# Kernel tuning notes

Measured on AMD Instinct MI355X. Metric: run time of the kernel, lower is better.

## Reference

```python
import jax, jax.numpy as jnp
import numpy as np

B, NODE, DEG, K = 16, 32, 64, 8
IN_F, OUT_F, SUP = 128, 3, 10
FEATS = [96, 256, 256, 256, 128, 128]
SIZES = [1, 2, 4, 8, 16, 32]


def setup_inputs() -> dict:
    key = jax.random.key(0)
    ks = jax.random.split(key, 20)
    d = {}
    for i in range(6):
        d[f"t{i}"] = jax.random.normal(ks[i], (B, SIZES[i], FEATS[i]), jnp.float32)
    for i in range(6):
        d[f"Wr{i}"] = jax.random.normal(ks[6 + i], (FEATS[i], OUT_F), jnp.float32) * 0.1
    d["W_branch"] = jax.random.normal(ks[12], (NODE, IN_F, DEG * IN_F), jnp.float32) * 0.02
    d["Wl1"] = jax.random.normal(ks[13], (IN_F, IN_F * SUP), jnp.float32) * 0.05
    d["Wl2"] = jax.random.normal(ks[14], (IN_F * SUP, OUT_F), jnp.float32) * 0.02
    d["bias"] = jax.random.uniform(ks[15], (1, DEG, OUT_F), jnp.float32, -0.5, 0.5)
    d["c1w"] = jax.random.normal(ks[16], (64, 6), jnp.float32) * 0.2
    d["c1b"] = jnp.zeros((64,), jnp.float32)
    d["c2w"] = jax.random.normal(ks[17], (3, 64), jnp.float32) * 0.1
    d["c2b"] = jnp.zeros((3,), jnp.float32)
    return d


def _leaky(x):
    return jnp.where(x >= 0, x, 0.2 * x)  # LeakyReLU(0.2)


def reference(t0, t1, t2, t3, t4, t5, Wr0, Wr1, Wr2, Wr3, Wr4, Wr5,
              W_branch, Wl1, Wl2, bias, c1w, c1b, c2w, c2b):
    trees = [t0, t1, t2, t3, t4, t5]
    Wrs = [Wr0, Wr1, Wr2, Wr3, Wr4, Wr5]

    # --- root aggregation: per-ancestor linear + contiguous tiling to `node` rows ---
    root = jnp.zeros((B, NODE, OUT_F), jnp.float32)
    for t, W in zip(trees, Wrs):
        rn = t.shape[1]
        root = root + jnp.repeat(t @ W, NODE // rn, axis=1)  # (B, NODE, 3)

    # --- branch upsample: per-node weight matrix, then 2-layer loop MLP ---
    branch = _leaky(jnp.einsum('bni,nio->bno', t5, W_branch))  # (B, NODE, DEG*IN_F)
    branch = branch.reshape(B, NODE * DEG, IN_F)
    branch = (branch @ Wl1) @ Wl2  # (B, N, 3)
    branch = jnp.repeat(root, DEG, axis=1) + branch  # (B, N, 3), N = NODE*DEG

    # --- EdgeConv: knn on 3-d points, gather, 1x1 convs, max over neighbors ---
    x = branch  # (B, N, 3) point coordinates
    xx = jnp.sum(x * x, axis=-1)  # (B, N)
    inner = jnp.einsum('bnc,bmc->bnm', x, x)  # (B, N, N)
    pd = 2.0 * inner - xx[:, :, None] - xx[:, None, :]  # -squared distance
    _, idx = jax.lax.top_k(pd, K)  # (B, N, K) nearest-neighbor indices

    feat = x[jnp.arange(B)[:, None, None], idx]  # (B, N, K, 3) gather
    center = jnp.broadcast_to(x[:, :, None, :], feat.shape)
    g = jnp.concatenate([feat - center, center], axis=-1)  # (B, N, K, 6)

    h = jnp.einsum('bnkc,oc->bnko', g, c1w) + c1b  # conv1 1x1: 6 -> 64
    h = jnp.einsum('bnko,po->bnkp', h, c2w) + c2b  # conv2 1x1: 64 -> 3
    h = jnp.max(h, axis=2)  # max over K neighbors -> (B, N, 3)

    out = _leaky(h + jnp.tile(bias, (1, NODE, 1)))  # bias (1, DEG, 3) tiled to (1, N, 3)
    return out
```

## Files before the change

kernel.cpp:

```cpp
#include <hip/hip_runtime.h>
#include <float.h>

#define B_    16
#define NODE_ 32
#define DEG_  64
#define KNN_  8
#define INF_  128
#define ROWS_ 2048
#define JDIM_ 8192

#define OFF_X     0
#define OFF_Y     131072
#define OFF_ROOT  (OFF_Y + 4194304)
#define OFF_WL12  (OFF_ROOT + 2048)
#define OFF_EFF   (OFF_WL12 + 512)

__device__ __forceinline__ float med3f(float a, float b, float c) {
    return __builtin_amdgcn_fmed3f(a, b, c);
}
__device__ __forceinline__ float leaky(float v) { return v >= 0.f ? v : 0.2f * v; }

__global__ __launch_bounds__(128) void kA(
    const float* __restrict__ t0, const float* __restrict__ t1, const float* __restrict__ t2,
    const float* __restrict__ t3, const float* __restrict__ t4, const float* __restrict__ t5,
    const float* __restrict__ Wr0, const float* __restrict__ Wr1, const float* __restrict__ Wr2,
    const float* __restrict__ Wr3, const float* __restrict__ Wr4, const float* __restrict__ Wr5,
    const float* __restrict__ Wl1, const float* __restrict__ Wl2,
    const float* __restrict__ c1w, const float* __restrict__ c1b,
    const float* __restrict__ c2w, const float* __restrict__ c2b,
    float* __restrict__ ws)
{
    const int blk = blockIdx.x, tid = threadIdx.x;
    if (blk == 0) {
        const float* wp = Wl1 + tid * 1280;
        float a0 = 0.f, a1 = 0.f, a2 = 0.f;
        for (int s = 0; s < 1280; ++s) {
            float w = wp[s];
            a0 = fmaf(w, Wl2[s * 3 + 0], a0);
            a1 = fmaf(w, Wl2[s * 3 + 1], a1);
            a2 = fmaf(w, Wl2[s * 3 + 2], a2);
        }
        float* o = ws + OFF_WL12 + tid * 4;
        o[0] = a0; o[1] = a1; o[2] = a2; o[3] = 0.f;
    } else if (blk <= 12) {
        int idx = (blk - 1) * 128 + tid;
        int c = idx % 3, n = (idx / 3) & 31, b = idx / 96;
        float acc = 0.f;
#define TREE(T, W, RN, F) { \
        const float* tp = T + (b * RN + ((n * RN) >> 5)) * F; \
        for (int k = 0; k < F; ++k) acc = fmaf(tp[k], W[k * 3 + c], acc); }
        TREE(t0, Wr0, 1, 96)
        TREE(t1, Wr1, 2, 256)
        TREE(t2, Wr2, 4, 256)
        TREE(t3, Wr3, 8, 256)
        TREE(t4, Wr4, 16, 128)
        TREE(t5, Wr5, 32, 128)
#undef TREE
        ws[OFF_ROOT + (b * 32 + n) * 4 + c] = acc;
    } else {
        if (tid < 18) {
            int p = tid / 6, c = tid % 6;
            float a = 0.f;
            for (int o = 0; o < 64; ++o) a = fmaf(c2w[p * 64 + o], c1w[o * 6 + c], a);
            ws[OFF_EFF + tid] = a;
        } else if (tid < 21) {
            int p = tid - 18;
            float a = c2b[p];
            for (int o = 0; o < 64; ++o) a = fmaf(c2w[p * 64 + o], c1b[o], a);
            ws[OFF_EFF + 24 + p] = a;
        }
    }
}

__global__ __launch_bounds__(256) void kB1(const float* __restrict__ t5,
                                           const float* __restrict__ Wb,
                                           float* __restrict__ ws)
{
    const int n = blockIdx.x >> 5, jt = blockIdx.x & 31, tid = threadIdx.x;
    __shared__ float ts[128 * 16];
    for (int q = tid; q < 2048; q += 256) {
        int b = q >> 7, k = q & 127;
        ts[k * 16 + b] = t5[b * 4096 + n * 128 + k];
    }
    __syncthreads();
    const int j = jt * 256 + tid;
    const float* wp = Wb + n * 1048576 + j;
    float acc[16];
#pragma unroll
    for (int b = 0; b < 16; ++b) acc[b] = 0.f;
#pragma unroll 4
    for (int k = 0; k < 128; ++k) {
        float w = wp[k * 8192];
        const float4* tk = (const float4*)(ts + (k << 4));
        float4 a0 = tk[0], a1 = tk[1], a2 = tk[2], a3 = tk[3];
        acc[0]  = fmaf(a0.x, w, acc[0]);  acc[1]  = fmaf(a0.y, w, acc[1]);
        acc[2]  = fmaf(a0.z, w, acc[2]);  acc[3]  = fmaf(a0.w, w, acc[3]);
        acc[4]  = fmaf(a1.x, w, acc[4]);  acc[5]  = fmaf(a1.y, w, acc[5]);
        acc[6]  = fmaf(a1.z, w, acc[6]);  acc[7]  = fmaf(a1.w, w, acc[7]);
        acc[8]  = fmaf(a2.x, w, acc[8]);  acc[9]  = fmaf(a2.y, w, acc[9]);
        acc[10] = fmaf(a2.z, w, acc[10]); acc[11] = fmaf(a2.w, w, acc[11]);
        acc[12] = fmaf(a3.x, w, acc[12]); acc[13] = fmaf(a3.y, w, acc[13]);
        acc[14] = fmaf(a3.z, w, acc[14]); acc[15] = fmaf(a3.w, w, acc[15]);
    }
    float* yp = ws + OFF_Y + n * 8192 + j;
#pragma unroll
    for (int b = 0; b < 16; ++b) yp[b * 262144] = leaky(acc[b]);
}

__global__ __launch_bounds__(256) void kB2(float* __restrict__ ws)
{
    __shared__ float wl[512];
    const int tid = threadIdx.x;
    for (int q = tid; q < 512; q += 256) wl[q] = ws[OFF_WL12 + q];
    __syncthreads();
    const int gid = blockIdx.x * 256 + tid;
    const int b = gid >> 11, r = gid & 2047, n = r >> 6;
    const float* rt = ws + OFF_ROOT + ((b * 32 + n) << 2);
    float x0 = rt[0], x1 = rt[1], x2 = rt[2];
    const float4* yp = (const float4*)(ws + OFF_Y + (size_t)(b * 32 + n) * 8192 + ((r & 63) << 7));
#pragma unroll 8
    for (int i4 = 0; i4 < 32; ++i4) {
        float4 y = yp[i4];
        const float4* wr = ((const float4*)wl) + (i4 << 2);
        float4 w0 = wr[0], w1 = wr[1], w2 = wr[2], w3 = wr[3];
        x0 = fmaf(y.x, w0.x, x0); x0 = fmaf(y.y, w1.x, x0); x0 = fmaf(y.z, w2.x, x0); x0 = fmaf(y.w, w3.x, x0);
        x1 = fmaf(y.x, w0.y, x1); x1 = fmaf(y.y, w1.y, x1); x1 = fmaf(y.z, w2.y, x1); x1 = fmaf(y.w, w3.y, x1);
        x2 = fmaf(y.x, w0.z, x2); x2 = fmaf(y.y, w1.z, x2); x2 = fmaf(y.z, w2.z, x2); x2 = fmaf(y.w, w3.z, x2);
    }
    float xx = fmaf(x0, x0, fmaf(x1, x1, x2 * x2));
    ((float4*)(ws + OFF_X))[gid] = make_float4(x0, x1, x2, xx);
}

#define CAP_ 16
#define CSWAPD(a, b) { float _hi = fmaxf(a, b), _lo = fminf(a, b); a = _hi; b = _lo; }
__global__ __launch_bounds__(256) void kC(const float* __restrict__ ws,
                                          const float* __restrict__ bias,
                                          float* __restrict__ out)
{
    const int bb = blockIdx.x >> 6, rtile = blockIdx.x & 63, tid = threadIdx.x;
    __shared__ float4 xs[2048];
    __shared__ float eff[32];
    __shared__ int cnt[32];
    __shared__ int lists[32][CAP_];
    __shared__ int sel[32][KNN_];

    const float4* xg = (const float4*)(ws + OFF_X) + bb * 2048;
    for (int q = tid; q < 2048; q += 256) xs[q] = xg[q];
    if (tid < 32) { eff[tid] = ws[OFF_EFF + tid]; cnt[tid] = 0; }
    __syncthreads();

    const int lr = tid >> 3;
    const int part = tid & 7;
    const int r = rtile * 32 + lr;
    const float4 xr = xs[r];

    float s0 = -FLT_MAX, s1 = -FLT_MAX, s2 = -FLT_MAX, s3 = -FLT_MAX;
    float s4 = -FLT_MAX, s5 = -FLT_MAX, s6 = -FLT_MAX, s7 = -FLT_MAX;
#pragma unroll 4
    for (int mm = 0; mm < 256; ++mm) {
        float4 xm = xs[(mm << 3) | part];
        float dot = fmaf(xr.x, xm.x, fmaf(xr.y, xm.y, xr.z * xm.z));
        float pd = fmaf(2.f, dot, -(xr.w + xm.w));
        s7 = med3f(pd, s7, s6); s6 = med3f(pd, s6, s5);
        s5 = med3f(pd, s5, s4); s4 = med3f(pd, s4, s3);
        s3 = med3f(pd, s3, s2); s2 = med3f(pd, s2, s1);
        s1 = med3f(pd, s1, s0); s0 = fmaxf(s0, pd);
    }
#pragma unroll
    for (int w = 1; w < 8; w <<= 1) {
        float o0 = __shfl_xor(s0, w), o1 = __shfl_xor(s1, w), o2 = __shfl_xor(s2, w), o3 = __shfl_xor(s3, w);
        float o4 = __shfl_xor(s4, w), o5 = __shfl_xor(s5, w), o6 = __shfl_xor(s6, w), o7 = __shfl_xor(s7, w);
        float n0 = fmaxf(s0, o7), n1 = fmaxf(s1, o6), n2 = fmaxf(s2, o5), n3 = fmaxf(s3, o4);
        float n4 = fmaxf(s4, o3), n5 = fmaxf(s5, o2), n6 = fmaxf(s6, o1), n7 = fmaxf(s7, o0);
        CSWAPD(n0, n4) CSWAPD(n1, n5) CSWAPD(n2, n6) CSWAPD(n3, n7)
        CSWAPD(n0, n2) CSWAPD(n1, n3) CSWAPD(n4, n6) CSWAPD(n5, n7)
        CSWAPD(n0, n1) CSWAPD(n2, n3) CSWAPD(n4, n5) CSWAPD(n6, n7)
        s0 = n0; s1 = n1; s2 = n2; s3 = n3; s4 = n4; s5 = n5; s6 = n6; s7 = n7;
    }
    const float T = s7;

#pragma unroll 4
    for (int mm = 0; mm < 256; ++mm) {
        int m = (mm << 3) | part;
        float4 xm = xs[m];
        float dot = fmaf(xr.x, xm.x, fmaf(xr.y, xm.y, xr.z * xm.z));
        float pd = fmaf(2.f, dot, -(xr.w + xm.w));
        if (pd >= T) {
            int slot = atomicAdd(&cnt[lr], 1);
            if (slot < CAP_) lists[lr][slot] = m | ((pd > T) ? 0x10000 : 0);
        }
    }
    __syncthreads();

    if (part == 0) {
        int c = cnt[lr]; if (c > CAP_) c = CAP_;
        int ng = 0;
        for (int q = 0; q < c; ++q) {
            int v = lists[lr][q];
            if (v & 0x10000) sel[lr][ng++] = v & 0xFFFF;
        }
        int prev = -1;
        while (ng < KNN_) {
            int best = 0x7FFFFFFF;
            for (int q = 0; q < c; ++q) {
                int v = lists[lr][q];
                if (!(v & 0x10000)) {
                    int m = v & 0xFFFF;
                    if (m > prev && m < best) best = m;
                }
            }
            if (best == 0x7FFFFFFF) best = r;
            sel[lr][ng++] = best; prev = best;
        }
    }
    __syncthreads();

    const int ms = sel[lr][part];
    const float4 fm = xs[ms];
    const float g0 = fm.x - xr.x, g1 = fm.y - xr.y, g2 = fm.z - xr.z;
    float h0 = eff[24], h1 = eff[25], h2 = eff[26];
    h0 = fmaf(g0, eff[0], h0);  h0 = fmaf(g1, eff[1], h0);  h0 = fmaf(g2, eff[2], h0);
    h0 = fmaf(xr.x, eff[3], h0); h0 = fmaf(xr.y, eff[4], h0); h0 = fmaf(xr.z, eff[5], h0);
    h1 = fmaf(g0, eff[6], h1);  h1 = fmaf(g1, eff[7], h1);  h1 = fmaf(g2, eff[8], h1);
    h1 = fmaf(xr.x, eff[9], h1); h1 = fmaf(xr.y, eff[10], h1); h1 = fmaf(xr.z, eff[11], h1);
    h2 = fmaf(g0, eff[12], h2); h2 = fmaf(g1, eff[13], h2); h2 = fmaf(g2, eff[14], h2);
    h2 = fmaf(xr.x, eff[15], h2); h2 = fmaf(xr.y, eff[16], h2); h2 = fmaf(xr.z, eff[17], h2);
#pragma unroll
    for (int w = 1; w < 8; w <<= 1) {
        h0 = fmaxf(h0, __shfl_xor(h0, w));
        h1 = fmaxf(h1, __shfl_xor(h1, w));
        h2 = fmaxf(h2, __shfl_xor(h2, w));
    }
    if (part == 0) {
        const float* bp = bias + (r & 63) * 3;
        float* op = out + (size_t)(bb * 2048 + r) * 3;
        op[0] = leaky(h0 + bp[0]);
        op[1] = leaky(h1 + bp[1]);
        op[2] = leaky(h2 + bp[2]);
    }
}

extern "C" void kernel_launch(void* const* d_in, const int* in_sizes, int n_in,
                              void* d_out, int out_size, void* d_ws, size_t ws_size,
                              hipStream_t stream)
{
    const float* t0 = (const float*)d_in[0];
    const float* t1 = (const float*)d_in[1];
    const float* t2 = (const float*)d_in[2];
    const float* t3 = (const float*)d_in[3];
    const float* t4 = (const float*)d_in[4];
    const float* t5 = (const float*)d_in[5];
    const float* Wr0 = (const float*)d_in[6];
    const float* Wr1 = (const float*)d_in[7];
    const float* Wr2 = (const float*)d_in[8];
    const float* Wr3 = (const float*)d_in[9];
    const float* Wr4 = (const float*)d_in[10];
    const float* Wr5 = (const float*)d_in[11];
    const float* Wb  = (const float*)d_in[12];
    const float* Wl1 = (const float*)d_in[13];
    const float* Wl2 = (const float*)d_in[14];
    const float* bias = (const float*)d_in[15];
    const float* c1w = (const float*)d_in[16];
    const float* c1b = (const float*)d_in[17];
    const float* c2w = (const float*)d_in[18];
    const float* c2b = (const float*)d_in[19];
    float* ws = (float*)d_ws;
    float* out = (float*)d_out;

    hipLaunchKernelGGL(kA, dim3(14), dim3(128), 0, stream,
                       t0, t1, t2, t3, t4, t5, Wr0, Wr1, Wr2, Wr3, Wr4, Wr5,
                       Wl1, Wl2, c1w, c1b, c2w, c2b, ws);
    hipLaunchKernelGGL(kB1, dim3(1024), dim3(256), 0, stream, t5, Wb, ws);
    hipLaunchKernelGGL(kB2, dim3(128), dim3(256), 0, stream, ws);
    hipLaunchKernelGGL(kC, dim3(1024), dim3(256), 0, stream, ws, bias, out);
}
```

Before: 354.7 us.

## Register-block kB1 over columns and batch, and kC over four query rows

kB1 now has each thread load a float4 of four adjacent weight columns and compute a 4x4 tile of outputs for a quarter of the batch, giving vectorized weight loads and stores instead of one scalar weight per thread. kC now gives each thread four query rows over a 1/32 slice of candidates, so every candidate point read from LDS is reused for four distance computations. The top-8 merge then spans 32 lanes instead of 8. The changes aim to cut memory and LDS traffic per FMA, at the cost of higher register pressure from 32 running top-k values in kC and more shuffle merge rounds.

```diff
diff --git a/kernel.cpp b/kernel.cpp
--- a/kernel.cpp
+++ b/kernel.cpp
@@ -5,9 +5,7 @@
 #define NODE_ 32
 #define DEG_  64
 #define KNN_  8
-#define INF_  128
 #define ROWS_ 2048
-#define JDIM_ 8192
 
 #define OFF_X     0
 #define OFF_Y     131072
@@ -83,28 +81,28 @@
         ts[k * 16 + b] = t5[b * 4096 + n * 128 + k];
     }
     __syncthreads();
-    const int j = jt * 256 + tid;
+    const int j  = jt * 256 + ((tid & 63) << 2);
+    const int bq = tid >> 6;
     const float* wp = Wb + n * 1048576 + j;
-    float acc[16];
-#pragma unroll
-    for (int b = 0; b < 16; ++b) acc[b] = 0.f;
+    float4 acc0 = {0,0,0,0}, acc1 = {0,0,0,0}, acc2 = {0,0,0,0}, acc3 = {0,0,0,0};
 #pragma unroll 4
     for (int k = 0; k < 128; ++k) {
-        float w = wp[k * 8192];
-        const float4* tk = (const float4*)(ts + (k << 4));
-        float4 a0 = tk[0], a1 = tk[1], a2 = tk[2], a3 = tk[3];
-        acc[0]  = fmaf(a0.x, w, acc[0]);  acc[1]  = fmaf(a0.y, w, acc[1]);
-        acc[2]  = fmaf(a0.z, w, acc[2]);  acc[3]  = fmaf(a0.w, w, acc[3]);
-        acc[4]  = fmaf(a1.x, w, acc[4]);  acc[5]  = fmaf(a1.y, w, acc[5]);
-        acc[6]  = fmaf(a1.z, w, acc[6]);  acc[7]  = fmaf(a1.w, w, acc[7]);
-        acc[8]  = fmaf(a2.x, w, acc[8]);  acc[9]  = fmaf(a2.y, w, acc[9]);
-        acc[10] = fmaf(a2.z, w, acc[10]); acc[11] = fmaf(a2.w, w, acc[11]);
-        acc[12] = fmaf(a3.x, w, acc[12]); acc[13] = fmaf(a3.y, w, acc[13]);
-        acc[14] = fmaf(a3.z, w, acc[14]); acc[15] = fmaf(a3.w, w, acc[15]);
-    }
-    float* yp = ws + OFF_Y + n * 8192 + j;
-#pragma unroll
-    for (int b = 0; b < 16; ++b) yp[b * 262144] = leaky(acc[b]);
+        float4 wv = *(const float4*)(wp + k * 8192);
+        float4 tb = *(const float4*)(ts + k * 16 + bq * 4);
+        acc0.x = fmaf(tb.x, wv.x, acc0.x); acc0.y = fmaf(tb.x, wv.y, acc0.y);
+        acc0.z = fmaf(tb.x, wv.z, acc0.z); acc0.w = fmaf(tb.x, wv.w, acc0.w);
+        acc1.x = fmaf(tb.y, wv.x, acc1.x); acc1.y = fmaf(tb.y, wv.y, acc1.y);
+        acc1.z = fmaf(tb.y, wv.z, acc1.z); acc1.w = fmaf(tb.y, wv.w, acc1.w);
+        acc2.x = fmaf(tb.z, wv.x, acc2.x); acc2.y = fmaf(tb.z, wv.y, acc2.y);
+        acc2.z = fmaf(tb.z, wv.z, acc2.z); acc2.w = fmaf(tb.z, wv.w, acc2.w);
+        acc3.x = fmaf(tb.w, wv.x, acc3.x); acc3.y = fmaf(tb.w, wv.y, acc3.y);
+        acc3.z = fmaf(tb.w, wv.z, acc3.z); acc3.w = fmaf(tb.w, wv.w, acc3.w);
+    }
+    float* yb = ws + OFF_Y + n * 8192 + j;
+#define STY(A, BI) { float4 y = make_float4(leaky(A.x), leaky(A.y), leaky(A.z), leaky(A.w)); \
+                     *(float4*)(yb + (size_t)(4 * bq + BI) * 262144) = y; }
+    STY(acc0, 0) STY(acc1, 1) STY(acc2, 2) STY(acc3, 3)
+#undef STY
 }
 
 __global__ __launch_bounds__(256) void kB2(float* __restrict__ ws)
@@ -133,6 +131,22 @@
 
 #define CAP_ 16
 #define CSWAPD(a, b) { float _hi = fmaxf(a, b), _lo = fminf(a, b); a = _hi; b = _lo; }
+#define INS8(P, s0,s1,s2,s3,s4,s5,s6,s7) \
+    s7 = med3f(P, s7, s6); s6 = med3f(P, s6, s5); \
+    s5 = med3f(P, s5, s4); s4 = med3f(P, s4, s3); \
+    s3 = med3f(P, s3, s2); s2 = med3f(P, s2, s1); \
+    s1 = med3f(P, s1, s0); s0 = fmaxf(s0, P);
+#define MERGE8(W, s0,s1,s2,s3,s4,s5,s6,s7) { \
+    float o0 = __shfl_xor(s0, W), o1 = __shfl_xor(s1, W), o2 = __shfl_xor(s2, W), o3 = __shfl_xor(s3, W); \
+    float o4 = __shfl_xor(s4, W), o5 = __shfl_xor(s5, W), o6 = __shfl_xor(s6, W), o7 = __shfl_xor(s7, W); \
+    float n0 = fmaxf(s0, o7), n1 = fmaxf(s1, o6), n2 = fmaxf(s2, o5), n3 = fmaxf(s3, o4); \
+    float n4 = fmaxf(s4, o3), n5 = fmaxf(s5, o2), n6 = fmaxf(s6, o1), n7 = fmaxf(s7, o0); \
+    CSWAPD(n0, n4) CSWAPD(n1, n5) CSWAPD(n2, n6) CSWAPD(n3, n7) \
+    CSWAPD(n0, n2) CSWAPD(n1, n3) CSWAPD(n4, n6) CSWAPD(n5, n7) \
+    CSWAPD(n0, n1) CSWAPD(n2, n3) CSWAPD(n4, n5) CSWAPD(n6, n7) \
+    s0 = n0; s1 = n1; s2 = n2; s3 = n3; s4 = n4; s5 = n5; s6 = n6; s7 = n7; }
+#define PD(XR, XM) fmaf(2.f, fmaf(XR.x, XM.x, fmaf(XR.y, XM.y, XR.z * XM.z)), -(XR.w + XM.w))
+
 __global__ __launch_bounds__(256) void kC(const float* __restrict__ ws,
                                           const float* __restrict__ bias,
                                           float* __restrict__ out)
@@ -149,49 +163,51 @@
     if (tid < 32) { eff[tid] = ws[OFF_EFF + tid]; cnt[tid] = 0; }
     __syncthreads();
 
+    const int g  = tid >> 5;
+    const int mp = tid & 31;
+    const int r0 = rtile * 32 + g * 4;
+    const float4 xa = xs[r0], xb = xs[r0 + 1], xc = xs[r0 + 2], xd = xs[r0 + 3];
+
+    float A0=-FLT_MAX,A1=-FLT_MAX,A2=-FLT_MAX,A3=-FLT_MAX,A4=-FLT_MAX,A5=-FLT_MAX,A6=-FLT_MAX,A7=-FLT_MAX;
+    float B0=-FLT_MAX,B1=-FLT_MAX,B2=-FLT_MAX,B3=-FLT_MAX,B4=-FLT_MAX,B5=-FLT_MAX,B6=-FLT_MAX,B7=-FLT_MAX;
+    float C0=-FLT_MAX,C1=-FLT_MAX,C2=-FLT_MAX,C3=-FLT_MAX,C4=-FLT_MAX,C5=-FLT_MAX,C6=-FLT_MAX,C7=-FLT_MAX;
+    float D0=-FLT_MAX,D1=-FLT_MAX,D2=-FLT_MAX,D3=-FLT_MAX,D4=-FLT_MAX,D5=-FLT_MAX,D6=-FLT_MAX,D7=-FLT_MAX;
+
+#pragma unroll 4
+    for (int mm = 0; mm < 64; ++mm) {
+        float4 xm = xs[(mm << 5) | mp];
+        float pa = PD(xa, xm); INS8(pa, A0,A1,A2,A3,A4,A5,A6,A7)
+        float pb = PD(xb, xm); INS8(pb, B0,B1,B2,B3,B4,B5,B6,B7)
+        float pc = PD(xc, xm); INS8(pc, C0,C1,C2,C3,C4,C5,C6,C7)
+        float pdv = PD(xd, xm); INS8(pdv, D0,D1,D2,D3,D4,D5,D6,D7)
+    }
+#pragma unroll
+    for (int w = 1; w < 32; w <<= 1) {
+        MERGE8(w, A0,A1,A2,A3,A4,A5,A6,A7)
+        MERGE8(w, B0,B1,B2,B3,B4,B5,B6,B7)
+        MERGE8(w, C0,C1,C2,C3,C4,C5,C6,C7)
+        MERGE8(w, D0,D1,D2,D3,D4,D5,D6,D7)
+    }
+    const float Ta = A7, Tb = B7, Tc = C7, Td = D7;
+
+#pragma unroll 4
+    for (int mm = 0; mm < 64; ++mm) {
+        int m = (mm << 5) | mp;
+        float4 xm = xs[m];
+        float pa = PD(xa, xm);
+        float pb = PD(xb, xm);
+        float pc = PD(xc, xm);
+        float pdv = PD(xd, xm);
+        if (pa >= Ta) { int s = atomicAdd(&cnt[g*4+0], 1); if (s < CAP_) lists[g*4+0][s] = m | ((pa > Ta) ? 0x10000 : 0); }
+        if (pb >= Tb) { int s = atomicAdd(&cnt[g*4+1], 1); if (s < CAP_) lists[g*4+1][s] = m | ((pb > Tb) ? 0x10000 : 0); }
+        if (pc >= Tc) { int s = atomicAdd(&cnt[g*4+2], 1); if (s < CAP_) lists[g*4+2][s] = m | ((pc > Tc) ? 0x10000 : 0); }
+        if (pdv >= Td){ int s = atomicAdd(&cnt[g*4+3], 1); if (s < CAP_) lists[g*4+3][s] = m | ((pdv > Td) ? 0x10000 : 0); }
+    }
+    __syncthreads();
+
     const int lr = tid >> 3;
     const int part = tid & 7;
     const int r = rtile * 32 + lr;
-    const float4 xr = xs[r];
-
-    float s0 = -FLT_MAX, s1 = -FLT_MAX, s2 = -FLT_MAX, s3 = -FLT_MAX;
-    float s4 = -FLT_MAX, s5 = -FLT_MAX, s6 = -FLT_MAX, s7 = -FLT_MAX;
-#pragma unroll 4
-    for (int mm = 0; mm < 256; ++mm) {
-        float4 xm = xs[(mm << 3) | part];
-        float dot = fmaf(xr.x, xm.x, fmaf(xr.y, xm.y, xr.z * xm.z));
-        float pd = fmaf(2.f, dot, -(xr.w + xm.w));
-        s7 = med3f(pd, s7, s6); s6 = med3f(pd, s6, s5);
-        s5 = med3f(pd, s5, s4); s4 = med3f(pd, s4, s3);
-        s3 = med3f(pd, s3, s2); s2 = med3f(pd, s2, s1);
-        s1 = med3f(pd, s1, s0); s0 = fmaxf(s0, pd);
-    }
-#pragma unroll
-    for (int w = 1; w < 8; w <<= 1) {
-        float o0 = __shfl_xor(s0, w), o1 = __shfl_xor(s1, w), o2 = __shfl_xor(s2, w), o3 = __shfl_xor(s3, w);
-        float o4 = __shfl_xor(s4, w), o5 = __shfl_xor(s5, w), o6 = __shfl_xor(s6, w), o7 = __shfl_xor(s7, w);
-        float n0 = fmaxf(s0, o7), n1 = fmaxf(s1, o6), n2 = fmaxf(s2, o5), n3 = fmaxf(s3, o4);
-        float n4 = fmaxf(s4, o3), n5 = fmaxf(s5, o2), n6 = fmaxf(s6, o1), n7 = fmaxf(s7, o0);
-        CSWAPD(n0, n4) CSWAPD(n1, n5) CSWAPD(n2, n6) CSWAPD(n3, n7)
-        CSWAPD(n0, n2) CSWAPD(n1, n3) CSWAPD(n4, n6) CSWAPD(n5, n7)
-        CSWAPD(n0, n1) CSWAPD(n2, n3) CSWAPD(n4, n5) CSWAPD(n6, n7)
-        s0 = n0; s1 = n1; s2 = n2; s3 = n3; s4 = n4; s5 = n5; s6 = n6; s7 = n7;
-    }
-    const float T = s7;
-
-#pragma unroll 4
-    for (int mm = 0; mm < 256; ++mm) {
-        int m = (mm << 3) | part;
-        float4 xm = xs[m];
-        float dot = fmaf(xr.x, xm.x, fmaf(xr.y, xm.y, xr.z * xm.z));
-        float pd = fmaf(2.f, dot, -(xr.w + xm.w));
-        if (pd >= T) {
-            int slot = atomicAdd(&cnt[lr], 1);
-            if (slot < CAP_) lists[lr][slot] = m | ((pd > T) ? 0x10000 : 0);
-        }
-    }
-    __syncthreads();
-
     if (part == 0) {
         int c = cnt[lr]; if (c > CAP_) c = CAP_;
         int ng = 0;
@@ -215,6 +231,7 @@
     }
     __syncthreads();
 
+    const float4 xr = xs[r];
     const int ms = sel[lr][part];
     const float4 fm = xs[ms];
     const float g0 = fm.x - xr.x, g1 = fm.y - xr.y, g2 = fm.z - xr.z;
```

Result: no change. 354.0 us (-0.2%).
